# Performance work log

Measured on AMD Instinct MI355X. Metric: run time of the kernel, lower is better.

Reference implementation:

```python
import jax, jax.numpy as jnp
import numpy as np

B, DIM1, DIM2, LATENT, T = 16, 1024, 1024, 512, 2048  # T == video_feat_dim
LN_EPS = 1e-5


def setup_inputs() -> dict:
    key = jax.random.key(0)
    ks = jax.random.split(key, 8)
    def xavier(k, shape):
        fan_out, fan_in = shape
        std = float(np.sqrt(2.0 / (fan_in + fan_out)))
        return jax.random.normal(k, shape, dtype=jnp.float32) * std
    return {
        "input1": jax.random.normal(ks[0], (B, DIM1, T), dtype=jnp.float32),
        "input2": jax.random.normal(ks[1], (B, DIM2, T), dtype=jnp.float32),
        "theta_w": xavier(ks[2], (LATENT, DIM2)),
        "theta_b": jnp.zeros((LATENT,), jnp.float32),
        "phi_w": xavier(ks[3], (LATENT, DIM1)),
        "phi_b": jnp.zeros((LATENT,), jnp.float32),
        "g_w": xavier(ks[4], (LATENT, DIM1)),
        "g_b": jnp.zeros((LATENT,), jnp.float32),
        "ln_gamma": jnp.ones((LATENT, T), jnp.float32),
        "ln_beta": jnp.zeros((LATENT, T), jnp.float32),
        "out_w": xavier(ks[5], (DIM2, LATENT)),
        "out_b": jnp.zeros((DIM2,), jnp.float32),
    }


def reference(input1, input2, theta_w, theta_b, phi_w, phi_b, g_w, g_b,
              ln_gamma, ln_beta, out_w, out_b):
    # 1x1 Conv1d == channel-wise matmul
    theta_x = jnp.einsum('ld,bdt->btl', theta_w, input2) + theta_b          # [B,T2,L]
    phi_x = jnp.einsum('ld,bdt->blt', phi_w, input1) + phi_b[:, None]       # [B,L,T1]
    scores = jnp.einsum('btl,bls->bts', theta_x, phi_x)                      # [B,T2,T1] (unscaled)
    p = jax.nn.softmax(scores, axis=-1)
    g_x = jnp.einsum('ld,bdt->btl', g_w, input1) + g_b                       # [B,T1,L]
    t_x = jnp.einsum('bts,bsl->blt', p, g_x)                                 # [B,L,T2]
    # LayerNorm over the last two dims jointly [LATENT, T]
    mu = jnp.mean(t_x, axis=(1, 2), keepdims=True)
    var = jnp.var(t_x, axis=(1, 2), keepdims=True)
    h = (t_x - mu) * jax.lax.rsqrt(var + LN_EPS) * ln_gamma + ln_beta
    h = jax.nn.relu(h)
    w_t = jnp.einsum('ol,blt->bot', out_w, h) + out_b[None, :, None]         # [B,DIM2,T2]
    return w_t + input2
```

## Files before the change

### kernel.cpp

```cpp
#include <hip/hip_runtime.h>
#include <hip/hip_bf16.h>

#define BB 16
#define D1 1024
#define D2 1024
#define LL 512
#define TT 2048
#define LN_EPS 1e-5f

typedef unsigned short u16;
typedef __attribute__((ext_vector_type(8))) _Float16 half8;
typedef __attribute__((ext_vector_type(4))) float f32x4;
typedef __attribute__((ext_vector_type(4))) unsigned int u32x4;

__device__ __forceinline__ u16 f2h(float v) {
    _Float16 h = (_Float16)v;
    return *(u16*)&h;
}
__device__ __forceinline__ float h2f(u16 u) {
    return (float)(*(const _Float16*)&u);
}

__device__ __forceinline__ void gload_lds16(const void* g, void* l) {
    __builtin_amdgcn_global_load_lds((const __attribute__((address_space(1))) void*)g,
                                     (__attribute__((address_space(3))) void*)l, 16, 0, 0);
}

#define MEMFENCE asm volatile("" ::: "memory")
__device__ __forceinline__ void block_barrier() {
    MEMFENCE; __builtin_amdgcn_s_barrier(); MEMFENCE;
}

template<int BIAS, int OMODE>
__global__ __launch_bounds__(512, 2) void nt_gemm(
    const u16* __restrict__ A, const u16* __restrict__ B,
    long sAb, long sBb, long sCb,
    int N, int Kd, int gx, int gy,
    const float* __restrict__ bias,
    void* __restrict__ out0,
    const float* __restrict__ resid, long sRb)
{
    __shared__ __align__(16) u16 smem[65536];

    const int nwg = gridDim.x;
    const int id = blockIdx.x;
    const int swz = (id & 7) * (nwg >> 3) + (id >> 3);
    const int bx = swz % gx;
    const int byz = swz / gx;
    const int by = byz % gy;
    const int b = byz / gy;

    const int tid = threadIdx.x;
    const long arow0 = (long)by * 256;
    const long brow0 = (long)bx * 256;
    const u16* Ab = A + (long)b * sAb + arow0 * Kd;
    const u16* Bb = B + (long)b * sBb + brow0 * Kd;

    const int wave = tid >> 6, lane = tid & 63;
    const int wm = (wave >> 2) * 128, wn = (wave & 3) * 64;
    const int lm = lane & 15, kg = lane >> 4;

    const int m0 = tid >> 3, s0 = tid & 7;
    const int nt = Kd >> 6;

    auto STAGE = [&](int buf, long k0) {
        u16* Ad = smem + buf * 32768;
        u16* Bd = smem + buf * 32768 + 16384;
#pragma unroll
        for (int call = 0; call < 4; ++call) {
            int m = call * 64 + m0;
            int gs = s0 ^ (m & 7);
            gload_lds16(Ab + k0 + (long)m * Kd + gs * 8, Ad + (call * 512 + tid) * 8);
        }
#pragma unroll
        for (int call = 0; call < 4; ++call) {
            int m = call * 64 + m0;
            int gs = s0 ^ (m & 7);
            gload_lds16(Bb + k0 + (long)m * Kd + gs * 8, Bd + (call * 512 + tid) * 8);
        }
    };

    f32x4 acc[8][4];
#pragma unroll
    for (int i = 0; i < 8; ++i)
#pragma unroll
        for (int j = 0; j < 4; ++j) acc[i][j] = (f32x4){0.f, 0.f, 0.f, 0.f};

    STAGE(0, 0);
    if (nt > 1) STAGE(1, 64);

    for (int t = 0; t < nt; ++t) {
        const int cur = t & 1;
        if (t + 1 < nt) { asm volatile("s_waitcnt vmcnt(8)" ::: "memory"); }
        else           { asm volatile("s_waitcnt vmcnt(0)" ::: "memory"); }
        block_barrier();

        const u16* Ac = smem + cur * 32768;
        const u16* Bc = smem + cur * 32768 + 16384;

        half8 bf[4][2];
#pragma unroll
        for (int f = 0; f < 4; ++f)
#pragma unroll
            for (int kf = 0; kf < 2; ++kf) {
                int nr = wn + f * 16 + lm;
                int ss = (kf * 4 + kg) ^ (nr & 7);
                bf[f][kf] = *(const half8*)(Bc + nr * 64 + ss * 8);
            }
#pragma unroll
        for (int mh = 0; mh < 2; ++mh) {
            half8 af[4][2];
#pragma unroll
            for (int f = 0; f < 4; ++f)
#pragma unroll
                for (int kf = 0; kf < 2; ++kf) {
                    int mr = wm + mh * 64 + f * 16 + lm;
                    int ss = (kf * 4 + kg) ^ (mr & 7);
                    af[f][kf] = *(const half8*)(Ac + mr * 64 + ss * 8);
                }
            __builtin_amdgcn_s_setprio(1);
#pragma unroll
            for (int f = 0; f < 4; ++f)
#pragma unroll
                for (int j = 0; j < 4; ++j)
#pragma unroll
                    for (int kf = 0; kf < 2; ++kf)
                        acc[mh * 4 + f][j] = __builtin_amdgcn_mfma_f32_16x16x32_f16(
                            af[f][kf], bf[j][kf], acc[mh * 4 + f][j], 0, 0, 0);
            __builtin_amdgcn_s_setprio(0);
        }
        block_barrier();
        if (t + 2 < nt) STAGE(cur, (long)(t + 2) * 64);
    }

    float* Cs = (float*)smem;
#pragma unroll
    for (int p = 0; p < 2; ++p) {
        __syncthreads();
        if (wm == p * 128) {
#pragma unroll
            for (int i = 0; i < 8; ++i)
#pragma unroll
                for (int j = 0; j < 4; ++j)
#pragma unroll
                    for (int r = 0; r < 4; ++r) {
                        int row = i * 16 + kg * 4 + r;
                        int col = wn + j * 16 + lm;
                        Cs[row * 256 + (col ^ ((row & 7) << 2))] = acc[i][j][r];
                    }
        }
        __syncthreads();
        if (OMODE == 0 || OMODE == 3) {
#pragma unroll
            for (int it = 0; it < 16; ++it) {
                int elem = it * 512 + tid;
                int row = elem >> 6, c4 = elem & 63;
                int grow = (int)arow0 + p * 128 + row;
                int gcol = (int)brow0 + c4 * 4;
                f32x4 v = *(const f32x4*)&Cs[row * 256 + ((c4 ^ (row & 7)) << 2)];
                if (BIAS == 1) v += bias[grow];
                if (BIAS == 2) v += *(const f32x4*)(bias + gcol);
                long off = (long)b * sCb + (long)grow * N + gcol;
                if (OMODE == 3) {
                    f32x4 rv = __builtin_nontemporal_load(
                        (const f32x4*)(resid + (long)b * sRb + (long)grow * N + gcol));
                    v += rv;
                }
                __builtin_nontemporal_store(v, (f32x4*)((float*)out0 + off));
            }
        } else {
#pragma unroll
            for (int it = 0; it < 8; ++it) {
                int elem = it * 512 + tid;
                int row = elem >> 5, c8 = elem & 31;
                int grow = (int)arow0 + p * 128 + row;
                int gcol = (int)brow0 + c8 * 8;
                int g0 = (c8 * 2) ^ (row & 7);
                int g1 = (c8 * 2 + 1) ^ (row & 7);
                f32x4 u0 = *(const f32x4*)&Cs[row * 256 + g0 * 4];
                f32x4 u1 = *(const f32x4*)&Cs[row * 256 + g1 * 4];
                float vv[8] = {u0.x, u0.y, u0.z, u0.w, u1.x, u1.y, u1.z, u1.w};
                if (BIAS == 1) {
                    float bb = bias[grow];
#pragma unroll
                    for (int q = 0; q < 8; ++q) vv[q] += bb;
                }
                if (BIAS == 2) {
#pragma unroll
                    for (int q = 0; q < 8; ++q) vv[q] += bias[gcol + q];
                }
                union { u16 u[8]; u32x4 v4; } pk;
#pragma unroll
                for (int q = 0; q < 8; ++q) pk.u[q] = f2h(vv[q]);
                long off = (long)b * sCb + (long)grow * N + gcol;
                __builtin_nontemporal_store(pk.v4, (u32x4*)((u16*)out0 + off));
            }
        }
    }
}

__global__ __launch_bounds__(256) void transpose_h(const float* __restrict__ in,
                                                   u16* __restrict__ o16, int D, int T) {
    __shared__ float tile[64][65];
    int b = blockIdx.z;
    const float* src = in + (long)b * D * T;
    long obase = (long)b * D * T;
    int t0 = blockIdx.x * 64, d0 = blockIdx.y * 64;
    int tx = threadIdx.x & 63, ty = threadIdx.x >> 6;
#pragma unroll
    for (int i = 0; i < 64; i += 4)
        tile[ty + i][tx] = __builtin_nontemporal_load(&src[(long)(d0 + ty + i) * T + t0 + tx]);
    __syncthreads();
#pragma unroll
    for (int i = 0; i < 64; i += 4) {
        long o = obase + (long)(t0 + ty + i) * D + d0 + tx;
        o16[o] = f2h(tile[tx][ty + i]);
    }
}

__global__ __launch_bounds__(256) void transpose_f32(const float* __restrict__ in,
                                                     float* __restrict__ out, int R, int C) {
    __shared__ float tile[64][65];
    int c0 = blockIdx.x * 64, r0 = blockIdx.y * 64;
    int tx = threadIdx.x & 63, ty = threadIdx.x >> 6;
#pragma unroll
    for (int i = 0; i < 64; i += 4)
        tile[ty + i][tx] = in[(long)(r0 + ty + i) * C + c0 + tx];
    __syncthreads();
#pragma unroll
    for (int i = 0; i < 64; i += 4)
        out[(long)(c0 + ty + i) * R + r0 + tx] = tile[tx][ty + i];
}

__global__ __launch_bounds__(256) void conv_w(const float* __restrict__ w,
                                              u16* __restrict__ h, int n) {
    int i = blockIdx.x * 256 + threadIdx.x;
    if (i < n) h[i] = f2h(w[i]);
}

__global__ __launch_bounds__(256) void softmax_rows(const float* __restrict__ S, u16* __restrict__ P) {
    long row = (long)blockIdx.z * TT + blockIdx.x;
    const float* s = S + row * TT;
    u16* p = P + row * TT;
    int tid = threadIdx.x;
    f32x4 v0 = __builtin_nontemporal_load((const f32x4*)(s + tid * 8));
    f32x4 v1 = __builtin_nontemporal_load((const f32x4*)(s + tid * 8 + 4));
    float x[8] = {v0.x, v0.y, v0.z, v0.w, v1.x, v1.y, v1.z, v1.w};
    float m = x[0];
#pragma unroll
    for (int j = 1; j < 8; ++j) m = fmaxf(m, x[j]);
#pragma unroll
    for (int off = 32; off; off >>= 1) m = fmaxf(m, __shfl_xor(m, off, 64));
    __shared__ float red[8];
    int wave = tid >> 6, lane = tid & 63;
    if (lane == 0) red[wave] = m;
    __syncthreads();
    m = fmaxf(fmaxf(red[0], red[1]), fmaxf(red[2], red[3]));
    float e[8]; float sum = 0.f;
#pragma unroll
    for (int j = 0; j < 8; ++j) { e[j] = __expf(x[j] - m); sum += e[j]; }
#pragma unroll
    for (int off = 32; off; off >>= 1) sum += __shfl_xor(sum, off, 64);
    if (lane == 0) red[4 + wave] = sum;
    __syncthreads();
    sum = red[4] + red[5] + red[6] + red[7];
    float inv = 1.f / sum;
    union { u16 u[8]; u32x4 v4; } pk;
#pragma unroll
    for (int j = 0; j < 8; ++j) pk.u[j] = f2h(e[j] * inv);
    *(u32x4*)(p + tid * 8) = pk.v4;
}

__global__ void zero32(float* p) { p[threadIdx.x] = 0.f; }

__global__ __launch_bounds__(256) void ln_partial(const u16* __restrict__ TXp, float* __restrict__ sums) {
    int b = blockIdx.z;
    const u16* x = TXp + (long)b * (LL * TT) + (long)blockIdx.x * 32768;
    int tid = threadIdx.x;
    float s = 0.f, sq = 0.f;
#pragma unroll 4
    for (int j = 0; j < 16; ++j) {
        u32x4 v = *(const u32x4*)(x + (j * 256 + tid) * 8);
        unsigned w[4] = {v.x, v.y, v.z, v.w};
#pragma unroll
        for (int q = 0; q < 4; ++q) {
            float a = h2f((u16)(w[q] & 0xffff));
            float c = h2f((u16)(w[q] >> 16));
            s += a + c;
            sq += a * a + c * c;
        }
    }
#pragma unroll
    for (int off = 32; off; off >>= 1) { s += __shfl_xor(s, off, 64); sq += __shfl_xor(sq, off, 64); }
    __shared__ float rs[8];
    int wave = tid >> 6, lane = tid & 63;
    if (lane == 0) { rs[wave] = s; rs[4 + wave] = sq; }
    __syncthreads();
    if (tid == 0) {
        atomicAdd(&sums[b * 2], rs[0] + rs[1] + rs[2] + rs[3]);
        atomicAdd(&sums[b * 2 + 1], rs[4] + rs[5] + rs[6] + rs[7]);
    }
}

__global__ __launch_bounds__(256) void ln_apply(const u16* __restrict__ TXp, const float* __restrict__ sums,
                                                const float* __restrict__ gT, const float* __restrict__ bT,
                                                u16* __restrict__ H) {
    int b = blockIdx.z;
    const float n = (float)(LL * TT);
    float mu = sums[b * 2] / n;
    float var = sums[b * 2 + 1] / n - mu * mu;
    float rstd = rsqrtf(var + LN_EPS);
    long base = (long)b * (LL * TT);
    long idx = ((long)blockIdx.x * 256 + threadIdx.x) * 8;
    u32x4 xv = *(const u32x4*)(TXp + base + idx);
    unsigned w[4] = {xv.x, xv.y, xv.z, xv.w};
    f32x4 g0 = *(const f32x4*)(gT + idx);
    f32x4 g1 = *(const f32x4*)(gT + idx + 4);
    f32x4 b0 = *(const f32x4*)(bT + idx);
    f32x4 b1 = *(const f32x4*)(bT + idx + 4);
    float g[8] = {g0.x, g0.y, g0.z, g0.w, g1.x, g1.y, g1.z, g1.w};
    float be[8] = {b0.x, b0.y, b0.z, b0.w, b1.x, b1.y, b1.z, b1.w};
    union { u16 u[8]; u32x4 v; } pk;
#pragma unroll
    for (int q = 0; q < 4; ++q) {
        float a = h2f((u16)(w[q] & 0xffff));
        float c = h2f((u16)(w[q] >> 16));
        float oa = fmaxf((a - mu) * rstd * g[q * 2] + be[q * 2], 0.f);
        float oc = fmaxf((c - mu) * rstd * g[q * 2 + 1] + be[q * 2 + 1], 0.f);
        pk.u[q * 2] = f2h(oa);
        pk.u[q * 2 + 1] = f2h(oc);
    }
    *(u32x4*)(H + base + idx) = pk.v;
}

extern "C" void kernel_launch(void* const* d_in, const int* in_sizes, int n_in,
                              void* d_out, int out_size, void* d_ws, size_t ws_size,
                              hipStream_t stream) {
    const float* input1  = (const float*)d_in[0];
    const float* input2  = (const float*)d_in[1];
    const float* theta_w = (const float*)d_in[2];
    const float* theta_b = (const float*)d_in[3];
    const float* phi_w   = (const float*)d_in[4];
    const float* phi_b   = (const float*)d_in[5];
    const float* g_w     = (const float*)d_in[6];
    const float* g_b     = (const float*)d_in[7];
    const float* ln_gamma= (const float*)d_in[8];
    const float* ln_beta = (const float*)d_in[9];
    const float* out_w   = (const float*)d_in[10];
    const float* out_b   = (const float*)d_in[11];
    float* out = (float*)d_out;

    char* ws = (char*)d_ws;
    const size_t MB = 1ull << 20;
    u16*  Xt     = (u16*)(ws + 0);
    float* scores= (float*)(ws + 0);
    u16*  pmat   = (u16*)(ws + 64 * MB);
    u16*  Qf     = (u16*)(ws + 192 * MB);
    u16*  Kf     = (u16*)(ws + 224 * MB);
    u16*  Vt     = (u16*)(ws + 256 * MB);
    u16*  TX     = (u16*)(ws + 288 * MB);
    u16*  H      = (u16*)(ws + 320 * MB);
    u16*  thw    = (u16*)(ws + 352 * MB);
    u16*  phw    = (u16*)(ws + 353 * MB);
    u16*  gww    = (u16*)(ws + 354 * MB);
    u16*  oww    = (u16*)(ws + 355 * MB);
    float* gammaT= (float*)(ws + 356 * MB);
    float* betaT = (float*)(ws + 360 * MB);
    float* sums  = (float*)(ws + 364 * MB);

    dim3 blk(256), blk5(512);

    conv_w<<<dim3((LL * D2 + 255) / 256), blk, 0, stream>>>(theta_w, thw, LL * D2);
    conv_w<<<dim3((LL * D1 + 255) / 256), blk, 0, stream>>>(phi_w, phw, LL * D1);
    conv_w<<<dim3((LL * D1 + 255) / 256), blk, 0, stream>>>(g_w, gww, LL * D1);
    conv_w<<<dim3((D2 * LL + 255) / 256), blk, 0, stream>>>(out_w, oww, D2 * LL);
    transpose_f32<<<dim3(TT / 64, LL / 64, 1), blk, 0, stream>>>(ln_gamma, gammaT, LL, TT);
    transpose_f32<<<dim3(TT / 64, LL / 64, 1), blk, 0, stream>>>(ln_beta, betaT, LL, TT);

    transpose_h<<<dim3(TT / 64, D2 / 64, BB), blk, 0, stream>>>(input2, Xt, D2, TT);
    nt_gemm<2, 1><<<dim3((LL / 256) * (TT / 256) * BB), blk5, 0, stream>>>(
        Xt, thw, (long)TT * D2, 0, (long)TT * LL, LL, D2, LL / 256, TT / 256,
        theta_b, Qf, nullptr, 0);

    transpose_h<<<dim3(TT / 64, D1 / 64, BB), blk, 0, stream>>>(input1, Xt, D1, TT);
    nt_gemm<2, 1><<<dim3((LL / 256) * (TT / 256) * BB), blk5, 0, stream>>>(
        Xt, phw, (long)TT * D1, 0, (long)TT * LL, LL, D1, LL / 256, TT / 256,
        phi_b, Kf, nullptr, 0);
    nt_gemm<1, 1><<<dim3((TT / 256) * (LL / 256) * BB), blk5, 0, stream>>>(
        gww, Xt, 0, (long)TT * D1, (long)LL * TT, TT, D1, TT / 256, LL / 256,
        g_b, Vt, nullptr, 0);

    for (int c = 0; c < 4; ++c) {
        long qoff = (long)c * 4 * TT * LL;
        nt_gemm<0, 0><<<dim3((TT / 256) * (TT / 256) * 4), blk5, 0, stream>>>(
            Qf + qoff, Kf + qoff, (long)TT * LL, (long)TT * LL, (long)TT * TT,
            TT, LL, TT / 256, TT / 256, nullptr, scores, nullptr, 0);
        softmax_rows<<<dim3(TT, 1, 4), blk, 0, stream>>>(scores, pmat + (long)c * 4 * TT * TT);
    }
    nt_gemm<0, 1><<<dim3((LL / 256) * (TT / 256) * BB), blk5, 0, stream>>>(
        pmat, Vt, (long)TT * TT, (long)LL * TT, (long)TT * LL,
        LL, TT, LL / 256, TT / 256, nullptr, TX, nullptr, 0);

    zero32<<<dim3(1), dim3(32), 0, stream>>>(sums);
    ln_partial<<<dim3(32, 1, BB), blk, 0, stream>>>(TX, sums);
    ln_apply<<<dim3(512, 1, BB), blk, 0, stream>>>(TX, sums, gammaT, betaT, H);

    nt_gemm<1, 3><<<dim3((TT / 256) * (D2 / 256) * BB), blk5, 0, stream>>>(
        oww, H, 0, (long)TT * LL, (long)D2 * TT, TT, LL, TT / 256, D2 / 256,
        out_b, out, input2, (long)D2 * TT);
}
```

Before: 585.6 us.

## Shrink GEMM tile to 256x128 with triple-buffered LDS pipeline

Changes the shared GEMM kernel from 256x256 output tiles to 256x128, with 8 waves arranged 4x2 and each wave computing a 64x64 sub-tile, so accumulator registers are halved. The K pipeline goes from double to triple buffering of LDS (144 KB), with adjusted vmcnt waits, and launch bounds drop to one block per CU. Intermediate stores and the softmax loads switch from nontemporal to normal accesses so the next kernel can hit in cache. The aim is more blocks to fill the CUs and deeper latency hiding, at the cost of lower arithmetic intensity per tile and less occupancy.

```diff
diff --git a/kernel.cpp b/kernel.cpp
--- a/kernel.cpp
+++ b/kernel.cpp
@@ -32,7 +32,7 @@
 }
 
 template<int BIAS, int OMODE>
-__global__ __launch_bounds__(512, 2) void nt_gemm(
+__global__ __launch_bounds__(512, 1) void nt_gemm(
     const u16* __restrict__ A, const u16* __restrict__ B,
     long sAb, long sBb, long sCb,
     int N, int Kd, int gx, int gy,
@@ -40,7 +40,7 @@
     void* __restrict__ out0,
     const float* __restrict__ resid, long sRb)
 {
-    __shared__ __align__(16) u16 smem[65536];
+    __shared__ __align__(16) u16 smem[73728];
 
     const int nwg = gridDim.x;
     const int id = blockIdx.x;
@@ -52,112 +52,109 @@
 
     const int tid = threadIdx.x;
     const long arow0 = (long)by * 256;
-    const long brow0 = (long)bx * 256;
+    const long brow0 = (long)bx * 128;
     const u16* Ab = A + (long)b * sAb + arow0 * Kd;
     const u16* Bb = B + (long)b * sBb + brow0 * Kd;
 
     const int wave = tid >> 6, lane = tid & 63;
-    const int wm = (wave >> 2) * 128, wn = (wave & 3) * 64;
+    const int wm = (wave >> 1) * 64, wn = (wave & 1) * 64;
     const int lm = lane & 15, kg = lane >> 4;
 
-    const int m0 = tid >> 3, s0 = tid & 7;
-    const int nt = Kd >> 6;
+    const int ntile = Kd >> 6;
 
     auto STAGE = [&](int buf, long k0) {
-        u16* Ad = smem + buf * 32768;
-        u16* Bd = smem + buf * 32768 + 16384;
+        u16* Ad = smem + buf * 24576;
+        u16* Bd = Ad + 16384;
 #pragma unroll
         for (int call = 0; call < 4; ++call) {
-            int m = call * 64 + m0;
-            int gs = s0 ^ (m & 7);
-            gload_lds16(Ab + k0 + (long)m * Kd + gs * 8, Ad + (call * 512 + tid) * 8);
+            int idx = call * 512 + tid;
+            int m = idx >> 3, s = idx & 7;
+            int gs = s ^ (m & 7);
+            gload_lds16(Ab + k0 + (long)m * Kd + gs * 8, Ad + idx * 8);
         }
 #pragma unroll
-        for (int call = 0; call < 4; ++call) {
-            int m = call * 64 + m0;
-            int gs = s0 ^ (m & 7);
-            gload_lds16(Bb + k0 + (long)m * Kd + gs * 8, Bd + (call * 512 + tid) * 8);
+        for (int call = 0; call < 2; ++call) {
+            int idx = call * 512 + tid;
+            int m = idx >> 3, s = idx & 7;
+            int gs = s ^ (m & 7);
+            gload_lds16(Bb + k0 + (long)m * Kd + gs * 8, Bd + idx * 8);
         }
     };
 
-    f32x4 acc[8][4];
-#pragma unroll
-    for (int i = 0; i < 8; ++i)
+    f32x4 acc[4][4];
+#pragma unroll
+    for (int i = 0; i < 4; ++i)
 #pragma unroll
         for (int j = 0; j < 4; ++j) acc[i][j] = (f32x4){0.f, 0.f, 0.f, 0.f};
 
     STAGE(0, 0);
-    if (nt > 1) STAGE(1, 64);
-
-    for (int t = 0; t < nt; ++t) {
-        const int cur = t & 1;
-        if (t + 1 < nt) { asm volatile("s_waitcnt vmcnt(8)" ::: "memory"); }
-        else           { asm volatile("s_waitcnt vmcnt(0)" ::: "memory"); }
+    if (ntile > 1) STAGE(1, 64);
+    if (ntile > 2) STAGE(2, 128);
+
+    for (int t = 0; t < ntile; ++t) {
+        const int cur = t % 3;
+        const int rem = ntile - 1 - t;
+        if (rem >= 2)      { asm volatile("s_waitcnt vmcnt(12)" ::: "memory"); }
+        else if (rem == 1) { asm volatile("s_waitcnt vmcnt(6)"  ::: "memory"); }
+        else               { asm volatile("s_waitcnt vmcnt(0)"  ::: "memory"); }
         block_barrier();
 
-        const u16* Ac = smem + cur * 32768;
-        const u16* Bc = smem + cur * 32768 + 16384;
-
-        half8 bf[4][2];
+        const u16* Ac = smem + cur * 24576;
+        const u16* Bc = Ac + 16384;
+
+        half8 af[4][2], bf[4][2];
 #pragma unroll
         for (int f = 0; f < 4; ++f)
 #pragma unroll
             for (int kf = 0; kf < 2; ++kf) {
                 int nr = wn + f * 16 + lm;
-                int ss = (kf * 4 + kg) ^ (nr & 7);
-                bf[f][kf] = *(const half8*)(Bc + nr * 64 + ss * 8);
+                int ssb = (kf * 4 + kg) ^ (nr & 7);
+                bf[f][kf] = *(const half8*)(Bc + nr * 64 + ssb * 8);
+                int mr = wm + f * 16 + lm;
+                int ssa = (kf * 4 + kg) ^ (mr & 7);
+                af[f][kf] = *(const half8*)(Ac + mr * 64 + ssa * 8);
             }
-#pragma unroll
-        for (int mh = 0; mh < 2; ++mh) {
-            half8 af[4][2];
-#pragma unroll
-            for (int f = 0; f < 4; ++f)
-#pragma unroll
-                for (int kf = 0; kf < 2; ++kf) {
-                    int mr = wm + mh * 64 + f * 16 + lm;
-                    int ss = (kf * 4 + kg) ^ (mr & 7);
-                    af[f][kf] = *(const half8*)(Ac + mr * 64 + ss * 8);
-                }
-            __builtin_amdgcn_s_setprio(1);
-#pragma unroll
-            for (int f = 0; f < 4; ++f)
-#pragma unroll
-                for (int j = 0; j < 4; ++j)
-#pragma unroll
-                    for (int kf = 0; kf < 2; ++kf)
-                        acc[mh * 4 + f][j] = __builtin_amdgcn_mfma_f32_16x16x32_f16(
-                            af[f][kf], bf[j][kf], acc[mh * 4 + f][j], 0, 0, 0);
-            __builtin_amdgcn_s_setprio(0);
-        }
+        __builtin_amdgcn_s_setprio(1);
+#pragma unroll
+        for (int i = 0; i < 4; ++i)
+#pragma unroll
+            for (int j = 0; j < 4; ++j)
+#pragma unroll
+                for (int kf = 0; kf < 2; ++kf)
+                    acc[i][j] = __builtin_amdgcn_mfma_f32_16x16x32_f16(
+                        af[i][kf], bf[j][kf], acc[i][j], 0, 0, 0);
+        __builtin_amdgcn_s_setprio(0);
+
         block_barrier();
-        if (t + 2 < nt) STAGE(cur, (long)(t + 2) * 64);
+        if (t + 3 < ntile) STAGE(cur, (long)(t + 3) * 64);
     }
 
     float* Cs = (float*)smem;
 #pragma unroll
     for (int p = 0; p < 2; ++p) {
         __syncthreads();
-        if (wm == p * 128) {
-#pragma unroll
-            for (int i = 0; i < 8; ++i)
+        if ((wave >> 2) == p) {
+            int rbase = (wave & 2) ? 64 : 0;
+#pragma unroll
+            for (int i = 0; i < 4; ++i)
 #pragma unroll
                 for (int j = 0; j < 4; ++j)
 #pragma unroll
                     for (int r = 0; r < 4; ++r) {
-                        int row = i * 16 + kg * 4 + r;
+                        int row = rbase + i * 16 + kg * 4 + r;
                         int col = wn + j * 16 + lm;
-                        Cs[row * 256 + (col ^ ((row & 7) << 2))] = acc[i][j][r];
+                        Cs[row * 128 + (col ^ ((row & 7) << 2))] = acc[i][j][r];
                     }
         }
         __syncthreads();
         if (OMODE == 0 || OMODE == 3) {
 #pragma unroll
-            for (int it = 0; it < 16; ++it) {
+            for (int it = 0; it < 8; ++it) {
                 int elem = it * 512 + tid;
-                int row = elem >> 6, c4 = elem & 63;
+                int row = elem >> 5, c4 = elem & 31;
                 int grow = (int)arow0 + p * 128 + row;
                 int gcol = (int)brow0 + c4 * 4;
-                f32x4 v = *(const f32x4*)&Cs[row * 256 + ((c4 ^ (row & 7)) << 2)];
+                f32x4 v = *(const f32x4*)&Cs[row * 128 + ((c4 ^ (row & 7)) << 2)];
                 if (BIAS == 1) v += bias[grow];
                 if (BIAS == 2) v += *(const f32x4*)(bias + gcol);
                 long off = (long)b * sCb + (long)grow * N + gcol;
@@ -165,20 +162,22 @@
                     f32x4 rv = __builtin_nontemporal_load(
                         (const f32x4*)(resid + (long)b * sRb + (long)grow * N + gcol));
                     v += rv;
+                    __builtin_nontemporal_store(v, (f32x4*)((float*)out0 + off));
+                } else {
+                    *(f32x4*)((float*)out0 + off) = v;
                 }
-                __builtin_nontemporal_store(v, (f32x4*)((float*)out0 + off));
             }
         } else {
 #pragma unroll
-            for (int it = 0; it < 8; ++it) {
+            for (int it = 0; it < 4; ++it) {
                 int elem = it * 512 + tid;
-                int row = elem >> 5, c8 = elem & 31;
+                int row = elem >> 4, c8 = elem & 15;
                 int grow = (int)arow0 + p * 128 + row;
                 int gcol = (int)brow0 + c8 * 8;
                 int g0 = (c8 * 2) ^ (row & 7);
                 int g1 = (c8 * 2 + 1) ^ (row & 7);
-                f32x4 u0 = *(const f32x4*)&Cs[row * 256 + g0 * 4];
-                f32x4 u1 = *(const f32x4*)&Cs[row * 256 + g1 * 4];
+                f32x4 u0 = *(const f32x4*)&Cs[row * 128 + g0 * 4];
+                f32x4 u1 = *(const f32x4*)&Cs[row * 128 + g1 * 4];
                 float vv[8] = {u0.x, u0.y, u0.z, u0.w, u1.x, u1.y, u1.z, u1.w};
                 if (BIAS == 1) {
                     float bb = bias[grow];
@@ -193,7 +192,7 @@
 #pragma unroll
                 for (int q = 0; q < 8; ++q) pk.u[q] = f2h(vv[q]);
                 long off = (long)b * sCb + (long)grow * N + gcol;
-                __builtin_nontemporal_store(pk.v4, (u32x4*)((u16*)out0 + off));
+                *(u32x4*)((u16*)out0 + off) = pk.v4;
             }
         }
     }
@@ -243,8 +242,8 @@
     const float* s = S + row * TT;
     u16* p = P + row * TT;
     int tid = threadIdx.x;
-    f32x4 v0 = __builtin_nontemporal_load((const f32x4*)(s + tid * 8));
-    f32x4 v1 = __builtin_nontemporal_load((const f32x4*)(s + tid * 8 + 4));
+    f32x4 v0 = *(const f32x4*)(s + tid * 8);
+    f32x4 v1 = *(const f32x4*)(s + tid * 8 + 4);
     float x[8] = {v0.x, v0.y, v0.z, v0.w, v1.x, v1.y, v1.z, v1.w};
     float m = x[0];
 #pragma unroll
@@ -378,34 +377,34 @@
     transpose_f32<<<dim3(TT / 64, LL / 64, 1), blk, 0, stream>>>(ln_beta, betaT, LL, TT);
 
     transpose_h<<<dim3(TT / 64, D2 / 64, BB), blk, 0, stream>>>(input2, Xt, D2, TT);
-    nt_gemm<2, 1><<<dim3((LL / 256) * (TT / 256) * BB), blk5, 0, stream>>>(
-        Xt, thw, (long)TT * D2, 0, (long)TT * LL, LL, D2, LL / 256, TT / 256,
+    nt_gemm<2, 1><<<dim3((LL / 128) * (TT / 256) * BB), blk5, 0, stream>>>(
+        Xt, thw, (long)TT * D2, 0, (long)TT * LL, LL, D2, LL / 128, TT / 256,
         theta_b, Qf, nullptr, 0);
 
     transpose_h<<<dim3(TT / 64, D1 / 64, BB), blk, 0, stream>>>(input1, Xt, D1, TT);
-    nt_gemm<2, 1><<<dim3((LL / 256) * (TT / 256) * BB), blk5, 0, stream>>>(
-        Xt, phw, (long)TT * D1, 0, (long)TT * LL, LL, D1, LL / 256, TT / 256,
+    nt_gemm<2, 1><<<dim3((LL / 128) * (TT / 256) * BB), blk5, 0, stream>>>(
+        Xt, phw, (long)TT * D1, 0, (long)TT * LL, LL, D1, LL / 128, TT / 256,
         phi_b, Kf, nullptr, 0);
-    nt_gemm<1, 1><<<dim3((TT / 256) * (LL / 256) * BB), blk5, 0, stream>>>(
-        gww, Xt, 0, (long)TT * D1, (long)LL * TT, TT, D1, TT / 256, LL / 256,
+    nt_gemm<1, 1><<<dim3((TT / 128) * (LL / 256) * BB), blk5, 0, stream>>>(
+        gww, Xt, 0, (long)TT * D1, (long)LL * TT, TT, D1, TT / 128, LL / 256,
         g_b, Vt, nullptr, 0);
 
     for (int c = 0; c < 4; ++c) {
         long qoff = (long)c * 4 * TT * LL;
-        nt_gemm<0, 0><<<dim3((TT / 256) * (TT / 256) * 4), blk5, 0, stream>>>(
+        nt_gemm<0, 0><<<dim3((TT / 128) * (TT / 256) * 4), blk5, 0, stream>>>(
             Qf + qoff, Kf + qoff, (long)TT * LL, (long)TT * LL, (long)TT * TT,
-            TT, LL, TT / 256, TT / 256, nullptr, scores, nullptr, 0);
+            TT, LL, TT / 128, TT / 256, nullptr, scores, nullptr, 0);
         softmax_rows<<<dim3(TT, 1, 4), blk, 0, stream>>>(scores, pmat + (long)c * 4 * TT * TT);
     }
-    nt_gemm<0, 1><<<dim3((LL / 256) * (TT / 256) * BB), blk5, 0, stream>>>(
+    nt_gemm<0, 1><<<dim3((LL / 128) * (TT / 256) * BB), blk5, 0, stream>>>(
         pmat, Vt, (long)TT * TT, (long)LL * TT, (long)TT * LL,
-        LL, TT, LL / 256, TT / 256, nullptr, TX, nullptr, 0);
+        LL, TT, LL / 128, TT / 256, nullptr, TX, nullptr, 0);
 
     zero32<<<dim3(1), dim3(32), 0, stream>>>(sums);
     ln_partial<<<dim3(32, 1, BB), blk, 0, stream>>>(TX, sums);
     ln_apply<<<dim3(512, 1, BB), blk, 0, stream>>>(TX, sums, gammaT, betaT, H);
 
-    nt_gemm<1, 3><<<dim3((TT / 256) * (D2 / 256) * BB), blk5, 0, stream>>>(
-        oww, H, 0, (long)TT * LL, (long)D2 * TT, TT, LL, TT / 256, D2 / 256,
+    nt_gemm<1, 3><<<dim3((TT / 128) * (D2 / 256) * BB), blk5, 0, stream>>>(
+        oww, H, 0, (long)TT * LL, (long)D2 * TT, TT, LL, TT / 128, D2 / 256,
         out_b, out, input2, (long)D2 * TT);
 }
```

After: 626.0 us. +6.9%, slower.

## Split GEMM K-step into four barrier-synchronized LDS-load/MFMA phases

Applied to the files above, without the earlier changes.

Restructures the GEMM main loop into four phases per K tile, each loading a smaller A or B fragment from LDS and then issuing a block of MFMAs between block barriers. The aim is to interleave LDS reads with MFMA work across waves and cut register pressure from holding all fragments at once. Launch bounds drop from two blocks to one per CU, giving more registers but less occupancy. Intermediate stores and the softmax loads now use normal instead of nontemporal accesses so the results can stay in cache for the next kernel. The extra barriers per tile could add synchronization overhead.

```diff
diff --git a/kernel.cpp b/kernel.cpp
--- a/kernel.cpp
+++ b/kernel.cpp
@@ -32,7 +32,7 @@
 }
 
 template<int BIAS, int OMODE>
-__global__ __launch_bounds__(512, 2) void nt_gemm(
+__global__ __launch_bounds__(512, 1) void nt_gemm(
     const u16* __restrict__ A, const u16* __restrict__ B,
     long sAb, long sBb, long sCb,
     int N, int Kd, int gx, int gy,
@@ -57,26 +57,29 @@
     const u16* Bb = B + (long)b * sBb + brow0 * Kd;
 
     const int wave = tid >> 6, lane = tid & 63;
-    const int wm = (wave >> 2) * 128, wn = (wave & 3) * 64;
+    const int mh = wave >> 2;
+    const int wm = mh * 128;
+    const int wn = (wave & 3) * 64;
     const int lm = lane & 15, kg = lane >> 4;
 
-    const int m0 = tid >> 3, s0 = tid & 7;
-    const int nt = Kd >> 6;
+    const int ntile = Kd >> 6;
 
     auto STAGE = [&](int buf, long k0) {
         u16* Ad = smem + buf * 32768;
-        u16* Bd = smem + buf * 32768 + 16384;
-#pragma unroll
-        for (int call = 0; call < 4; ++call) {
-            int m = call * 64 + m0;
-            int gs = s0 ^ (m & 7);
-            gload_lds16(Ab + k0 + (long)m * Kd + gs * 8, Ad + (call * 512 + tid) * 8);
+        u16* Bd = Ad + 16384;
+#pragma unroll
+        for (int sw = 0; sw < 4; ++sw) {
+            int idx = sw * 512 + tid;
+            int m = idx >> 3, s = idx & 7;
+            int gs = s ^ (m & 7);
+            gload_lds16(Ab + k0 + (long)m * Kd + gs * 8, Ad + idx * 8);
         }
 #pragma unroll
-        for (int call = 0; call < 4; ++call) {
-            int m = call * 64 + m0;
-            int gs = s0 ^ (m & 7);
-            gload_lds16(Bb + k0 + (long)m * Kd + gs * 8, Bd + (call * 512 + tid) * 8);
+        for (int sw = 0; sw < 4; ++sw) {
+            int idx = sw * 512 + tid;
+            int m = idx >> 3, s = idx & 7;
+            int gs = s ^ (m & 7);
+            gload_lds16(Bb + k0 + (long)m * Kd + gs * 8, Bd + idx * 8);
         }
     };
 
@@ -87,67 +90,74 @@
         for (int j = 0; j < 4; ++j) acc[i][j] = (f32x4){0.f, 0.f, 0.f, 0.f};
 
     STAGE(0, 0);
-    if (nt > 1) STAGE(1, 64);
-
-    for (int t = 0; t < nt; ++t) {
-        const int cur = t & 1;
-        if (t + 1 < nt) { asm volatile("s_waitcnt vmcnt(8)" ::: "memory"); }
-        else           { asm volatile("s_waitcnt vmcnt(0)" ::: "memory"); }
+    if (ntile > 1) STAGE(1, 64);
+
+    half8 a_[4][2], b_[2][2];
+
+#define LOADA(ms_) do { \
+    _Pragma("unroll") for (int f = 0; f < 4; ++f) \
+    _Pragma("unroll") for (int kf = 0; kf < 2; ++kf) { \
+        int mr = wm + (ms_) * 64 + f * 16 + lm; \
+        int ss = (kf * 4 + kg) ^ (mr & 7); \
+        a_[f][kf] = *(const half8*)(Ac + mr * 64 + ss * 8); } } while (0)
+#define LOADB(ns_) do { \
+    _Pragma("unroll") for (int f = 0; f < 2; ++f) \
+    _Pragma("unroll") for (int kf = 0; kf < 2; ++kf) { \
+        int nr = wn + (ns_) * 32 + f * 16 + lm; \
+        int ss = (kf * 4 + kg) ^ (nr & 7); \
+        b_[f][kf] = *(const half8*)(Bc + nr * 64 + ss * 8); } } while (0)
+#define PH_MFMA(ms_, ns_) do { \
+    block_barrier(); \
+    asm volatile("s_waitcnt lgkmcnt(0)" ::: "memory"); \
+    __builtin_amdgcn_sched_barrier(0); \
+    __builtin_amdgcn_s_setprio(1); \
+    _Pragma("unroll") for (int i = 0; i < 4; ++i) \
+    _Pragma("unroll") for (int j = 0; j < 2; ++j) \
+    _Pragma("unroll") for (int kf = 0; kf < 2; ++kf) \
+        acc[(ms_) * 4 + i][(ns_) * 2 + j] = __builtin_amdgcn_mfma_f32_16x16x32_f16( \
+            a_[i][kf], b_[j][kf], acc[(ms_) * 4 + i][(ns_) * 2 + j], 0, 0, 0); \
+    __builtin_amdgcn_s_setprio(0); \
+    block_barrier(); \
+} while (0)
+
+    for (int t = 0; t < ntile; ++t) {
+        const int c = t & 1;
+        const u16* Ac = smem + c * 32768;
+        const u16* Bc = Ac + 16384;
+        if (t + 1 < ntile) { asm volatile("s_waitcnt vmcnt(8)" ::: "memory"); }
+        else               { asm volatile("s_waitcnt vmcnt(0)" ::: "memory"); }
         block_barrier();
 
-        const u16* Ac = smem + cur * 32768;
-        const u16* Bc = smem + cur * 32768 + 16384;
-
-        half8 bf[4][2];
-#pragma unroll
-        for (int f = 0; f < 4; ++f)
-#pragma unroll
-            for (int kf = 0; kf < 2; ++kf) {
-                int nr = wn + f * 16 + lm;
-                int ss = (kf * 4 + kg) ^ (nr & 7);
-                bf[f][kf] = *(const half8*)(Bc + nr * 64 + ss * 8);
-            }
-#pragma unroll
-        for (int mh = 0; mh < 2; ++mh) {
-            half8 af[4][2];
-#pragma unroll
-            for (int f = 0; f < 4; ++f)
-#pragma unroll
-                for (int kf = 0; kf < 2; ++kf) {
-                    int mr = wm + mh * 64 + f * 16 + lm;
-                    int ss = (kf * 4 + kg) ^ (mr & 7);
-                    af[f][kf] = *(const half8*)(Ac + mr * 64 + ss * 8);
-                }
-            __builtin_amdgcn_s_setprio(1);
-#pragma unroll
-            for (int f = 0; f < 4; ++f)
-#pragma unroll
-                for (int j = 0; j < 4; ++j)
-#pragma unroll
-                    for (int kf = 0; kf < 2; ++kf)
-                        acc[mh * 4 + f][j] = __builtin_amdgcn_mfma_f32_16x16x32_f16(
-                            af[f][kf], bf[j][kf], acc[mh * 4 + f][j], 0, 0, 0);
-            __builtin_amdgcn_s_setprio(0);
-        }
-        block_barrier();
-        if (t + 2 < nt) STAGE(cur, (long)(t + 2) * 64);
-    }
+        LOADA(0); LOADB(0); PH_MFMA(0, 0);
+        LOADA(1);           PH_MFMA(1, 0);
+        LOADB(1);           PH_MFMA(1, 1);
+        LOADA(0);           PH_MFMA(0, 1);
+
+        if (t + 2 < ntile) STAGE(c, (long)(t + 2) * 64);
+    }
+#undef LOADA
+#undef LOADB
+#undef PH_MFMA
 
     float* Cs = (float*)smem;
 #pragma unroll
     for (int p = 0; p < 2; ++p) {
         __syncthreads();
-        if (wm == p * 128) {
-#pragma unroll
-            for (int i = 0; i < 8; ++i)
-#pragma unroll
-                for (int j = 0; j < 4; ++j)
-#pragma unroll
-                    for (int r = 0; r < 4; ++r) {
-                        int row = i * 16 + kg * 4 + r;
-                        int col = wn + j * 16 + lm;
-                        Cs[row * 256 + (col ^ ((row & 7) << 2))] = acc[i][j][r];
-                    }
+        if (mh == p) {
+#pragma unroll
+            for (int ms = 0; ms < 2; ++ms)
+#pragma unroll
+                for (int i = 0; i < 4; ++i)
+#pragma unroll
+                    for (int ns = 0; ns < 2; ++ns)
+#pragma unroll
+                        for (int j = 0; j < 2; ++j)
+#pragma unroll
+                            for (int r = 0; r < 4; ++r) {
+                                int row = ms * 64 + i * 16 + kg * 4 + r;
+                                int col = wn + ns * 32 + j * 16 + lm;
+                                Cs[row * 256 + (col ^ ((row & 7) << 2))] = acc[ms * 4 + i][ns * 2 + j][r];
+                            }
         }
         __syncthreads();
         if (OMODE == 0 || OMODE == 3) {
@@ -165,8 +175,10 @@
                     f32x4 rv = __builtin_nontemporal_load(
                         (const f32x4*)(resid + (long)b * sRb + (long)grow * N + gcol));
                     v += rv;
+                    __builtin_nontemporal_store(v, (f32x4*)((float*)out0 + off));
+                } else {
+                    *(f32x4*)((float*)out0 + off) = v;
                 }
-                __builtin_nontemporal_store(v, (f32x4*)((float*)out0 + off));
             }
         } else {
 #pragma unroll
@@ -193,7 +205,7 @@
 #pragma unroll
                 for (int q = 0; q < 8; ++q) pk.u[q] = f2h(vv[q]);
                 long off = (long)b * sCb + (long)grow * N + gcol;
-                __builtin_nontemporal_store(pk.v4, (u32x4*)((u16*)out0 + off));
+                *(u32x4*)((u16*)out0 + off) = pk.v4;
             }
         }
     }
@@ -243,8 +255,8 @@
     const float* s = S + row * TT;
     u16* p = P + row * TT;
     int tid = threadIdx.x;
-    f32x4 v0 = __builtin_nontemporal_load((const f32x4*)(s + tid * 8));
-    f32x4 v1 = __builtin_nontemporal_load((const f32x4*)(s + tid * 8 + 4));
+    f32x4 v0 = *(const f32x4*)(s + tid * 8);
+    f32x4 v1 = *(const f32x4*)(s + tid * 8 + 4);
     float x[8] = {v0.x, v0.y, v0.z, v0.w, v1.x, v1.y, v1.z, v1.w};
     float m = x[0];
 #pragma unroll
```

Result: slower. 603.3 us (+3.0%).
